# Optimization experiments

Measured on AMD Instinct MI355X. Metric: run time of the kernel, lower is better.

Reference implementation:

```python
import jax, jax.numpy as jnp
import numpy as np

N_LVL = [131072, 32768, 8192, 2048, 512, 256]  # active voxels per pyramid level
B = 8          # point clouds in batch
K = 27         # 3x3x3 kernel offsets
SLOPE = 0.01   # LeakyReLU default negative slope
EPS = 1e-5     # BatchNorm eps


def _bn(x, g, b):
    # MinkowskiBatchNorm, training-mode forward: stats over all points
    m = x.mean(0)
    v = x.var(0)
    return (x - m) * jax.lax.rsqrt(v + EPS) * g + b


def _lrelu(x):
    return jnp.where(x >= 0, x, SLOPE * x)


def _lin_block(x, w, g, b):
    # MinkowskiLinear(bias=False) + BN + LeakyReLU (also models 1x1 conv)
    return _lrelu(_bn(x @ w, g, b))


def _conv_block(x, nbr, w, g, b):
    # sparse conv as gather-GEMM: [N,K,Cin] x [K,Cin,Cout] -> [N,Cout]
    y = jnp.einsum('nkc,kco->no', x[nbr], w)
    return _lrelu(_bn(y, g, b))


def _maxpool(x, pmap):
    # stride-2 kernel-3 sparse max pool via precomputed pooling map
    return x[pmap].max(axis=1)


def setup_inputs() -> dict:
    key = jax.random.key(0)
    ks = iter(jax.random.split(key, 80))

    def nrm(shape, scale):
        return jax.random.normal(next(ks), shape, dtype=jnp.float32) * jnp.float32(scale)

    inp = {}
    inp['x'] = nrm((N_LVL[0], 3), 1.0)
    inp['w_mlp1'] = nrm((3, 16), 1.0 / np.sqrt(3.0))
    inp['g_mlp1'] = jnp.ones(16, jnp.float32)
    inp['b_mlp1'] = jnp.zeros(16, jnp.float32)
    conv_dims = [(16, 32), (32, 48), (48, 96), (96, 128), (128, 256), (256, 512)]
    down_dims = [(48, 32), (80, 48), (144, 96), (224, 128), (384, 256)]
    for i, (ci, co) in enumerate(conv_dims):
        inp[f'w_c{i+1}'] = nrm((K, ci, co), np.sqrt(2.0 / (K * co)))  # kaiming fan_out
        inp[f'g_c{i+1}'] = jnp.ones(co, jnp.float32)
        inp[f'b_c{i+1}'] = jnp.zeros(co, jnp.float32)
    for i, (ci, co) in enumerate(down_dims):
        inp[f'w_d{i+1}'] = nrm((ci, co), np.sqrt(2.0 / co))
        inp[f'g_d{i+1}'] = jnp.ones(co, jnp.float32)
        inp[f'b_d{i+1}'] = jnp.zeros(co, jnp.float32)
    inp['w_f1'] = nrm((1024, 512), 1.0 / 32.0)
    inp['g_f1'] = jnp.ones(512, jnp.float32)
    inp['b_f1'] = jnp.zeros(512, jnp.float32)
    inp['w_f2'] = nrm((512, 256), 1.0 / np.sqrt(512.0))
    inp['g_f2'] = jnp.ones(256, jnp.float32)
    inp['b_f2'] = jnp.zeros(256, jnp.float32)
    inp['w_f3'] = nrm((256, 20), 1.0 / 16.0)
    inp['bias_f3'] = jnp.zeros(20, jnp.float32)
    for i in range(6):
        inp[f'nbr{i}'] = jax.random.randint(next(ks), (N_LVL[i], K), 0, N_LVL[i], dtype=jnp.int32)
    for i in range(1, 6):
        inp[f'pool{i}'] = jax.random.randint(next(ks), (N_LVL[i], K), 0, N_LVL[i - 1], dtype=jnp.int32)
    inp['batch5'] = jnp.repeat(jnp.arange(B, dtype=jnp.int32), N_LVL[5] // B)
    return inp


def reference(x, w_mlp1, g_mlp1, b_mlp1,
              w_c1, g_c1, b_c1, w_c2, g_c2, b_c2, w_c3, g_c3, b_c3,
              w_c4, g_c4, b_c4, w_c5, g_c5, b_c5, w_c6, g_c6, b_c6,
              w_d1, g_d1, b_d1, w_d2, g_d2, b_d2, w_d3, g_d3, b_d3,
              w_d4, g_d4, b_d4, w_d5, g_d5, b_d5,
              w_f1, g_f1, b_f1, w_f2, g_f2, b_f2, w_f3, bias_f3,
              nbr0, nbr1, nbr2, nbr3, nbr4, nbr5,
              pool1, pool2, pool3, pool4, pool5, batch5):
    convs = [(w_c1, g_c1, b_c1), (w_c2, g_c2, b_c2), (w_c3, g_c3, b_c3),
             (w_c4, g_c4, b_c4), (w_c5, g_c5, b_c5)]
    downs = [(w_d1, g_d1, b_d1), (w_d2, g_d2, b_d2), (w_d3, g_d3, b_d3),
             (w_d4, g_d4, b_d4), (w_d5, g_d5, b_d5)]
    nbrs = [nbr0, nbr1, nbr2, nbr3, nbr4]
    pools = [pool1, pool2, pool3, pool4, pool5]

    y = _lin_block(x, w_mlp1, g_mlp1, b_mlp1)  # mlp1, level 0
    for i in range(5):  # fixed 5 conv/cat/down/pool stages (structural loop)
        out = _conv_block(y, nbrs[i], *convs[i])
        y = _lin_block(jnp.concatenate([y, out], axis=1), *downs[i])  # cat + down (1x1)
        y = _maxpool(y, pools[i])
    y = _conv_block(y, nbr5, w_c6, g_c6, b_c6)  # conv6 at level 5: [N5, 512]

    xmax = jax.ops.segment_max(y, batch5, num_segments=B)
    cnt = jax.ops.segment_sum(jnp.ones((y.shape[0], 1), y.dtype), batch5, num_segments=B)
    xavg = jax.ops.segment_sum(y, batch5, num_segments=B) / cnt
    z = jnp.concatenate([xmax, xavg], axis=1)  # [B, 1024]

    z = _lin_block(z, w_f1, g_f1, b_f1)  # dropout = identity (eval)
    z = _lin_block(z, w_f2, g_f2, b_f2)
    return z @ w_f3 + bias_f3  # [B, 20] logits
```

## Files before the change

kernel.cpp:

```cpp
#include <hip/hip_runtime.h>
#include <math.h>

#define BN_EPS 1e-5f


__device__ __forceinline__ void fma4(float s, const float4& w, float4& a) {
    a.x = fmaf(s, w.x, a.x);
    a.y = fmaf(s, w.y, a.y);
    a.z = fmaf(s, w.z, a.z);
    a.w = fmaf(s, w.w, a.w);
}

__device__ __forceinline__ float nlr(float x, float sc, float sh) {
    float t = fmaf(x, sc, sh);
    return fmaxf(t, 0.01f * t);
}

__device__ __forceinline__ void bn_coef(const float* __restrict__ sums,
                                        const float* __restrict__ g,
                                        const float* __restrict__ b,
                                        int C, int c, float inv_n,
                                        float& sc, float& sh) {
    float mean = sums[c] * inv_n;
    float var = fmaxf(fmaf(-mean, mean, sums[C + c] * inv_n), 0.f);
    sc = g[c] * rsqrtf(var + BN_EPS);
    sh = fmaf(-mean, sc, b[c]);
}

__global__ void zero_kernel(float* __restrict__ p, int n) {
    int i = blockIdx.x * blockDim.x + threadIdx.x;
    if (i < n) p[i] = 0.f;
}

__global__ __launch_bounds__(256) void mlp1s_kernel(
    const float* __restrict__ x, const float* __restrict__ w,
    float* __restrict__ out, int N, float* __restrict__ sums) {
    __shared__ float ls[32];
    int tid = threadIdx.x;
    if (tid < 32) ls[tid] = 0.f;
    __syncthreads();
    int n = blockIdx.x * blockDim.x + tid;
    float o[16];
    if (n < N) {
        float x0 = x[n * 3], x1 = x[n * 3 + 1], x2 = x[n * 3 + 2];
        #pragma unroll
        for (int c = 0; c < 16; c++)
            o[c] = fmaf(x0, w[c], fmaf(x1, w[16 + c], x2 * w[32 + c]));
        #pragma unroll
        for (int c4 = 0; c4 < 4; c4++)
            *reinterpret_cast<float4*>(out + n * 16 + c4 * 4) =
                make_float4(o[c4 * 4], o[c4 * 4 + 1], o[c4 * 4 + 2], o[c4 * 4 + 3]);
    } else {
        #pragma unroll
        for (int c = 0; c < 16; c++) o[c] = 0.f;
    }
    float q[16];
    #pragma unroll
    for (int c = 0; c < 16; c++) q[c] = o[c] * o[c];
    #pragma unroll
    for (int m = 1; m < 64; m <<= 1) {
        #pragma unroll
        for (int c = 0; c < 16; c++) {
            o[c] += __shfl_xor(o[c], m, 64);
            q[c] += __shfl_xor(q[c], m, 64);
        }
    }
    if ((tid & 63) == 0) {
        #pragma unroll
        for (int c = 0; c < 16; c++) {
            atomicAdd(&ls[c], o[c]);
            atomicAdd(&ls[16 + c], q[c]);
        }
    }
    __syncthreads();
    if (tid < 32) atomicAdd(&sums[tid], ls[tid]);
}

__global__ void norm0_kernel(float4* __restrict__ y, int total4,
                             const float* __restrict__ sums, const float* __restrict__ g,
                             const float* __restrict__ b, float inv_n) {
    __shared__ float lsc[16], lsh[16];
    int tid = threadIdx.x;
    if (tid < 16) {
        float sc, sh;
        bn_coef(sums, g, b, 16, tid, inv_n, sc, sh);
        lsc[tid] = sc;
        lsh[tid] = sh;
    }
    __syncthreads();
    int i = blockIdx.x * blockDim.x + tid;
    if (i >= total4) return;
    int cb = (i & 3) * 4;
    float4 v = y[i];
    v.x = nlr(v.x, lsc[cb + 0], lsh[cb + 0]);
    v.y = nlr(v.y, lsc[cb + 1], lsh[cb + 1]);
    v.z = nlr(v.z, lsc[cb + 2], lsh[cb + 2]);
    v.w = nlr(v.w, lsc[cb + 3], lsh[cb + 3]);
    y[i] = v;
}

__global__ void stats4_kernel(const float4* __restrict__ x, int total4, int C, int C4,
                              float* __restrict__ sums) {
    __shared__ float ls[1024];
    int tid = threadIdx.x;
    for (int j = tid; j < 2 * C; j += blockDim.x) ls[j] = 0.f;
    __syncthreads();
    int stride = gridDim.x * blockDim.x;
    int i = blockIdx.x * blockDim.x + tid;
    int c4 = i % C4;
    float4 s = make_float4(0.f, 0.f, 0.f, 0.f);
    float4 q = make_float4(0.f, 0.f, 0.f, 0.f);
    for (; i < total4; i += stride) {
        float4 v = x[i];
        s.x += v.x; s.y += v.y; s.z += v.z; s.w += v.w;
        q.x = fmaf(v.x, v.x, q.x); q.y = fmaf(v.y, v.y, q.y);
        q.z = fmaf(v.z, v.z, q.z); q.w = fmaf(v.w, v.w, q.w);
    }
    int cb = c4 * 4;
    atomicAdd(&ls[cb + 0], s.x); atomicAdd(&ls[cb + 1], s.y);
    atomicAdd(&ls[cb + 2], s.z); atomicAdd(&ls[cb + 3], s.w);
    atomicAdd(&ls[C + cb + 0], q.x); atomicAdd(&ls[C + cb + 1], q.y);
    atomicAdd(&ls[C + cb + 2], q.z); atomicAdd(&ls[C + cb + 3], q.w);
    __syncthreads();
    for (int j = tid; j < 2 * C; j += blockDim.x) atomicAdd(&sums[j], ls[j]);
}

template <int C, int KS>
__global__ void reducek_kernel(const float4* __restrict__ in, float4* __restrict__ out,
                               int total4, float* __restrict__ sums) {
    __shared__ float ls[1024];
    constexpr int C4 = C / 4;
    int tid = threadIdx.x;
    for (int j = tid; j < 2 * C; j += blockDim.x) ls[j] = 0.f;
    __syncthreads();
    int stride = gridDim.x * blockDim.x;
    int i = blockIdx.x * blockDim.x + tid;
    int c4 = i % C4;
    float4 s = make_float4(0.f, 0.f, 0.f, 0.f);
    float4 q = make_float4(0.f, 0.f, 0.f, 0.f);
    for (; i < total4; i += stride) {
        float4 v = make_float4(0.f, 0.f, 0.f, 0.f);
        #pragma unroll
        for (int p = 0; p < KS; p++) {
            float4 t = in[(size_t)p * total4 + i];
            v.x += t.x; v.y += t.y; v.z += t.z; v.w += t.w;
        }
        out[i] = v;
        s.x += v.x; s.y += v.y; s.z += v.z; s.w += v.w;
        q.x = fmaf(v.x, v.x, q.x); q.y = fmaf(v.y, v.y, q.y);
        q.z = fmaf(v.z, v.z, q.z); q.w = fmaf(v.w, v.w, q.w);
    }
    int cb = c4 * 4;
    atomicAdd(&ls[cb + 0], s.x); atomicAdd(&ls[cb + 1], s.y);
    atomicAdd(&ls[cb + 2], s.z); atomicAdd(&ls[cb + 3], s.w);
    atomicAdd(&ls[C + cb + 0], q.x); atomicAdd(&ls[C + cb + 1], q.y);
    atomicAdd(&ls[C + cb + 2], q.z); atomicAdd(&ls[C + cb + 3], q.w);
    __syncthreads();
    for (int j = tid; j < 2 * C; j += blockDim.x) atomicAdd(&sums[j], ls[j]);
}

template <int CIN, int COUT, int CO_TILE, int NCOT, int MT, int TM, int NTHR,
          int NQ, int KT, bool STATS, bool PREF>
__global__ __launch_bounds__(NTHR) void convd_kernel(
    const float* __restrict__ y, const int* __restrict__ nbr,
    const float* __restrict__ w, float* __restrict__ out,
    float* __restrict__ s_out) {
    constexpr int CQT = CO_TILE / (4 * NQ);
    constexpr int MGRP = NTHR / CQT;
    constexpr int RT = TM / MGRP;
    constexpr int C4N = CIN / 4;
    static_assert(MGRP * RT == TM, "tile mismatch");
    static_assert(MGRP * CQT == NTHR, "thread mismatch");

    __shared__ float sred[STATS ? 2 * CO_TILE : 1];

    const int tid = threadIdx.x;
    const int bid = blockIdx.x;
    const int cot = bid % NCOT;
    const int rest = bid / NCOT;
    const int mt = rest % MT;
    const int ks = rest / MT;
    const int m0 = mt * TM;
    const int cobase = cot * CO_TILE;
    const int k0 = ks * KT;
    const int cq = tid % CQT;
    const int mg = tid / CQT;

    int mrow[RT];
    #pragma unroll
    for (int r = 0; r < RT; r++) mrow[r] = m0 + mg + r * MGRP;

    float4 acc[RT][NQ];
    #pragma unroll
    for (int r = 0; r < RT; r++)
        #pragma unroll
        for (int q = 0; q < NQ; q++) acc[r][q] = make_float4(0.f, 0.f, 0.f, 0.f);

    auto ldidx = [&](int k, int (&rr)[RT]) {
        #pragma unroll
        for (int r = 0; r < RT; r++) rr[r] = nbr[(size_t)mrow[r] * 27 + k];
    };

    if constexpr (PREF) {
        auto ldy = [&](const int (&rr)[RT], float4 (&yv)[RT][C4N]) {
            #pragma unroll
            for (int r = 0; r < RT; r++)
                #pragma unroll
                for (int c4 = 0; c4 < C4N; c4++)
                    yv[r][c4] = *reinterpret_cast<const float4*>(
                        y + (size_t)rr[r] * CIN + c4 * 4);
        };
        auto fmak = [&](int k, const float4 (&yv)[RT][C4N]) {
            const float* wk = w + (size_t)k * CIN * COUT + cobase + cq * (4 * NQ);
            #pragma unroll
            for (int c4 = 0; c4 < C4N; c4++) {
                #pragma unroll
                for (int jj = 0; jj < 4; jj++) {
                    #pragma unroll
                    for (int q = 0; q < NQ; q++) {
                        float4 wv = *reinterpret_cast<const float4*>(
                            wk + (size_t)(c4 * 4 + jj) * COUT + q * 4);
                        #pragma unroll
                        for (int r = 0; r < RT; r++) {
                            float e = jj == 0 ? yv[r][c4].x : jj == 1 ? yv[r][c4].y
                                     : jj == 2 ? yv[r][c4].z : yv[r][c4].w;
                            fma4(e, wv, acc[r][q]);
                        }
                    }
                }
            }
        };
        int ra[RT], rb[RT];
        float4 ya[RT][C4N], yb[RT][C4N];
        ldidx(k0, ra);
        ldy(ra, ya);
        int kk = 0;
        for (; kk + 2 <= KT; kk += 2) {
            ldidx(k0 + kk + 1, rb);
            ldy(rb, yb);
            fmak(k0 + kk, ya);
            if (kk + 2 < KT) {
                ldidx(k0 + kk + 2, ra);
                ldy(ra, ya);
            }
            fmak(k0 + kk + 1, yb);
        }
        if (KT & 1) fmak(k0 + KT - 1, ya);
    } else {
        int rows[RT];
        ldidx(k0, rows);
        for (int kk = k0; kk < k0 + KT; kk++) {
            int rnext[RT];
            if (kk + 1 < k0 + KT) ldidx(kk + 1, rnext);
            const float* wk = w + (size_t)kk * CIN * COUT + cobase + cq * (4 * NQ);
            #pragma unroll 4
            for (int c4 = 0; c4 < C4N; c4++) {
                float4 yv[RT];
                #pragma unroll
                for (int r = 0; r < RT; r++)
                    yv[r] = *reinterpret_cast<const float4*>(
                        y + (size_t)rows[r] * CIN + c4 * 4);
                #pragma unroll
                for (int jj = 0; jj < 4; jj++) {
                    #pragma unroll
                    for (int q = 0; q < NQ; q++) {
                        float4 wv = *reinterpret_cast<const float4*>(
                            wk + (size_t)(c4 * 4 + jj) * COUT + q * 4);
                        #pragma unroll
                        for (int r = 0; r < RT; r++) {
                            float e = jj == 0 ? yv[r].x : jj == 1 ? yv[r].y
                                     : jj == 2 ? yv[r].z : yv[r].w;
                            fma4(e, wv, acc[r][q]);
                        }
                    }
                }
            }
            #pragma unroll
            for (int r = 0; r < RT; r++) rows[r] = rnext[r];
        }
    }

    float* outp = out + (size_t)ks * MT * TM * COUT;
    #pragma unroll
    for (int r = 0; r < RT; r++)
        #pragma unroll
        for (int q = 0; q < NQ; q++)
            *reinterpret_cast<float4*>(
                outp + (size_t)mrow[r] * COUT + cobase + cq * (4 * NQ) + q * 4) =
                acc[r][q];

    if constexpr (STATS) {
        for (int j = tid; j < 2 * CO_TILE; j += NTHR) sred[j] = 0.f;
        __syncthreads();
        #pragma unroll
        for (int q = 0; q < NQ; q++) {
            float4 s = make_float4(0.f, 0.f, 0.f, 0.f);
            float4 qq = make_float4(0.f, 0.f, 0.f, 0.f);
            #pragma unroll
            for (int r = 0; r < RT; r++) {
                float4 v = acc[r][q];
                s.x += v.x; s.y += v.y; s.z += v.z; s.w += v.w;
                qq.x = fmaf(v.x, v.x, qq.x); qq.y = fmaf(v.y, v.y, qq.y);
                qq.z = fmaf(v.z, v.z, qq.z); qq.w = fmaf(v.w, v.w, qq.w);
            }
            int cb = cq * (4 * NQ) + q * 4;
            atomicAdd(&sred[cb + 0], s.x); atomicAdd(&sred[cb + 1], s.y);
            atomicAdd(&sred[cb + 2], s.z); atomicAdd(&sred[cb + 3], s.w);
            atomicAdd(&sred[CO_TILE + cb + 0], qq.x);
            atomicAdd(&sred[CO_TILE + cb + 1], qq.y);
            atomicAdd(&sred[CO_TILE + cb + 2], qq.z);
            atomicAdd(&sred[CO_TILE + cb + 3], qq.w);
        }
        __syncthreads();
        for (int j = tid; j < CO_TILE; j += NTHR) {
            atomicAdd(&s_out[cobase + j], sred[j]);
            atomicAdd(&s_out[COUT + cobase + j], sred[CO_TILE + j]);
        }
    }
}

template <int C1, int C2, int COUT, int NQ, int NTHR>
__global__ __launch_bounds__(NTHR) void down3_kernel(
    const float* __restrict__ in1, const float* __restrict__ in2,
    const float* __restrict__ w, float* __restrict__ out,
    const float* __restrict__ s2, const float* __restrict__ g2,
    const float* __restrict__ b2, float inv2,
    float* __restrict__ s_out) {
    constexpr int CQT = COUT / (4 * NQ);
    constexpr int PAIRS = NTHR / CQT;
    __shared__ __align__(16) float n2c[C2], n2h[C2];
    __shared__ float sred[2 * COUT];

    const int tid = threadIdx.x;
    for (int c = tid; c < C2; c += NTHR) {
        float sc, sh;
        bn_coef(s2, g2, b2, C2, c, inv2, sc, sh);
        n2c[c] = sc; n2h[c] = sh;
    }
    for (int j = tid; j < 2 * COUT; j += NTHR) sred[j] = 0.f;
    __syncthreads();

    const int cq = tid % CQT;
    const int pr = tid / CQT;
    const int n0 = (blockIdx.x * PAIRS + pr) * 2;

    float4 acc[2][NQ];
    #pragma unroll
    for (int r = 0; r < 2; r++)
        #pragma unroll
        for (int q = 0; q < NQ; q++) acc[r][q] = make_float4(0.f, 0.f, 0.f, 0.f);

    const float* w1 = w + cq * (4 * NQ);
    #pragma unroll 8
    for (int ci4 = 0; ci4 < C1 / 4; ci4++) {
        float4 a0 = *reinterpret_cast<const float4*>(in1 + (size_t)n0 * C1 + ci4 * 4);
        float4 a1 = *reinterpret_cast<const float4*>(in1 + (size_t)(n0 + 1) * C1 + ci4 * 4);
        #pragma unroll
        for (int jj = 0; jj < 4; jj++) {
            const float* wp = w1 + (size_t)(ci4 * 4 + jj) * COUT;
            float e0 = jj == 0 ? a0.x : jj == 1 ? a0.y : jj == 2 ? a0.z : a0.w;
            float e1 = jj == 0 ? a1.x : jj == 1 ? a1.y : jj == 2 ? a1.z : a1.w;
            #pragma unroll
            for (int q = 0; q < NQ; q++) {
                float4 wv = *reinterpret_cast<const float4*>(wp + q * 4);
                fma4(e0, wv, acc[0][q]);
                fma4(e1, wv, acc[1][q]);
            }
        }
    }
    const float* w2 = w + (size_t)C1 * COUT + cq * (4 * NQ);
    #pragma unroll 8
    for (int ci4 = 0; ci4 < C2 / 4; ci4++) {
        float4 a0 = *reinterpret_cast<const float4*>(in2 + (size_t)n0 * C2 + ci4 * 4);
        float4 a1 = *reinterpret_cast<const float4*>(in2 + (size_t)(n0 + 1) * C2 + ci4 * 4);
        float4 sc = *reinterpret_cast<const float4*>(&n2c[ci4 * 4]);
        float4 sh = *reinterpret_cast<const float4*>(&n2h[ci4 * 4]);
        a0.x = nlr(a0.x, sc.x, sh.x); a0.y = nlr(a0.y, sc.y, sh.y);
        a0.z = nlr(a0.z, sc.z, sh.z); a0.w = nlr(a0.w, sc.w, sh.w);
        a1.x = nlr(a1.x, sc.x, sh.x); a1.y = nlr(a1.y, sc.y, sh.y);
        a1.z = nlr(a1.z, sc.z, sh.z); a1.w = nlr(a1.w, sc.w, sh.w);
        #pragma unroll
        for (int jj = 0; jj < 4; jj++) {
            const float* wp = w2 + (size_t)(ci4 * 4 + jj) * COUT;
            float e0 = jj == 0 ? a0.x : jj == 1 ? a0.y : jj == 2 ? a0.z : a0.w;
            float e1 = jj == 0 ? a1.x : jj == 1 ? a1.y : jj == 2 ? a1.z : a1.w;
            #pragma unroll
            for (int q = 0; q < NQ; q++) {
                float4 wv = *reinterpret_cast<const float4*>(wp + q * 4);
                fma4(e0, wv, acc[0][q]);
                fma4(e1, wv, acc[1][q]);
            }
        }
    }
    #pragma unroll
    for (int r = 0; r < 2; r++)
        #pragma unroll
        for (int q = 0; q < NQ; q++)
            *reinterpret_cast<float4*>(out + (size_t)(n0 + r) * COUT + cq * (4 * NQ) + q * 4) =
                acc[r][q];

    #pragma unroll
    for (int q = 0; q < NQ; q++) {
        float4 s = make_float4(0.f, 0.f, 0.f, 0.f);
        float4 qq = make_float4(0.f, 0.f, 0.f, 0.f);
        #pragma unroll
        for (int r = 0; r < 2; r++) {
            float4 v = acc[r][q];
            s.x += v.x; s.y += v.y; s.z += v.z; s.w += v.w;
            qq.x = fmaf(v.x, v.x, qq.x); qq.y = fmaf(v.y, v.y, qq.y);
            qq.z = fmaf(v.z, v.z, qq.z); qq.w = fmaf(v.w, v.w, qq.w);
        }
        int cb = cq * (4 * NQ) + q * 4;
        atomicAdd(&sred[cb + 0], s.x); atomicAdd(&sred[cb + 1], s.y);
        atomicAdd(&sred[cb + 2], s.z); atomicAdd(&sred[cb + 3], s.w);
        atomicAdd(&sred[COUT + cb + 0], qq.x);
        atomicAdd(&sred[COUT + cb + 1], qq.y);
        atomicAdd(&sred[COUT + cb + 2], qq.z);
        atomicAdd(&sred[COUT + cb + 3], qq.w);
    }
    __syncthreads();
    for (int j = tid; j < COUT; j += NTHR) {
        atomicAdd(&s_out[j], sred[j]);
        atomicAdd(&s_out[COUT + j], sred[COUT + j]);
    }
}

template <int C, int NTHR>
__global__ __launch_bounds__(NTHR) void pool2_kernel(
    const float* __restrict__ draw, const int* __restrict__ pmap,
    const float* __restrict__ sums, const float* __restrict__ g,
    const float* __restrict__ b, float inv_n,
    float* __restrict__ yout, int Nout) {
    constexpr int C4 = C / 4;
    int i = blockIdx.x * NTHR + threadIdx.x;
    if (i >= Nout * C4) return;
    int n = i / C4, c4 = i % C4;
    float sc[4], sh[4];
    #pragma unroll
    for (int j = 0; j < 4; j++) bn_coef(sums, g, b, C, c4 * 4 + j, inv_n, sc[j], sh[j]);
    const int* pm = pmap + n * 27;
    float4 mn = make_float4(INFINITY, INFINITY, INFINITY, INFINITY);
    float4 mx = make_float4(-INFINITY, -INFINITY, -INFINITY, -INFINITY);
    #pragma unroll 9
    for (int k = 0; k < 27; k++) {
        int row = pm[k];
        float4 v = *reinterpret_cast<const float4*>(draw + (size_t)row * C + c4 * 4);
        mn.x = fminf(mn.x, v.x); mn.y = fminf(mn.y, v.y);
        mn.z = fminf(mn.z, v.z); mn.w = fminf(mn.w, v.w);
        mx.x = fmaxf(mx.x, v.x); mx.y = fmaxf(mx.y, v.y);
        mx.z = fmaxf(mx.z, v.z); mx.w = fmaxf(mx.w, v.w);
    }
    float4 o;
    o.x = nlr(sc[0] >= 0.f ? mx.x : mn.x, sc[0], sh[0]);
    o.y = nlr(sc[1] >= 0.f ? mx.y : mn.y, sc[1], sh[1]);
    o.z = nlr(sc[2] >= 0.f ? mx.z : mn.z, sc[2], sh[2]);
    o.w = nlr(sc[3] >= 0.f ? mx.w : mn.w, sc[3], sh[3]);
    *reinterpret_cast<float4*>(yout + (size_t)n * C + c4 * 4) = o;
}

__global__ void segpool2_kernel(const float* __restrict__ y,
                                const float* __restrict__ sums,
                                const float* __restrict__ g, const float* __restrict__ b,
                                float inv_n, float* __restrict__ z) {
    int bi = blockIdx.x;
    int c = threadIdx.x;
    float sc, sh;
    bn_coef(sums, g, b, 512, c, inv_n, sc, sh);
    float mn = INFINITY, mx = -INFINITY, sm = 0.f;
    for (int r = 0; r < 32; r++) {
        float v = y[(size_t)(bi * 32 + r) * 512 + c];
        mn = fminf(mn, v);
        mx = fmaxf(mx, v);
        sm += nlr(v, sc, sh);
    }
    z[bi * 1024 + c] = nlr(sc >= 0.f ? mx : mn, sc, sh);
    z[bi * 1024 + 512 + c] = sm * (1.f / 32.f);
}

template <int K, int COUT, int KSPLIT, bool NORM>
__global__ __launch_bounds__(256) void fc_kernel(
    const float* __restrict__ z, const float* __restrict__ w,
    const float* __restrict__ ns, const float* __restrict__ ng,
    const float* __restrict__ nb, float inv_n,
    float* __restrict__ out) {
    constexpr int KC = K / KSPLIT;
    constexpr int KG = KC / 16;
    __shared__ __align__(16) float zt[KC * 8];
    __shared__ float red[16 * 520];

    const int cobase = blockIdx.x * 64;
    const int kc0 = blockIdx.y * KC;
    const int tid = threadIdx.x;
    const int coq = tid & 15;
    const int kg = tid >> 4;

    for (int idx = tid; idx < 8 * (KC / 4); idx += 256) {
        int n = idx / (KC / 4);
        int kq = idx - n * (KC / 4);
        float4 v = *reinterpret_cast<const float4*>(z + (size_t)n * K + kc0 + kq * 4);
        if constexpr (NORM) {
            #pragma unroll
            for (int j = 0; j < 4; j++) {
                float sc, sh;
                bn_coef(ns, ng, nb, K, kc0 + kq * 4 + j, inv_n, sc, sh);
                float* pv = j == 0 ? &v.x : j == 1 ? &v.y : j == 2 ? &v.z : &v.w;
                *pv = nlr(*pv, sc, sh);
            }
        }
        zt[(kq * 4 + 0) * 8 + n] = v.x;
        zt[(kq * 4 + 1) * 8 + n] = v.y;
        zt[(kq * 4 + 2) * 8 + n] = v.z;
        zt[(kq * 4 + 3) * 8 + n] = v.w;
    }
    __syncthreads();

    float4 acc[8];
    #pragma unroll
    for (int n = 0; n < 8; n++) acc[n] = make_float4(0.f, 0.f, 0.f, 0.f);
    for (int ki = 0; ki < KG; ki++) {
        int k = kg * KG + ki;
        float4 wv = *reinterpret_cast<const float4*>(
            w + (size_t)(kc0 + k) * COUT + cobase + coq * 4);
        float4 za = *reinterpret_cast<const float4*>(&zt[k * 8]);
        float4 zb = *reinterpret_cast<const float4*>(&zt[k * 8 + 4]);
        fma4(za.x, wv, acc[0]); fma4(za.y, wv, acc[1]);
        fma4(za.z, wv, acc[2]); fma4(za.w, wv, acc[3]);
        fma4(zb.x, wv, acc[4]); fma4(zb.y, wv, acc[5]);
        fma4(zb.z, wv, acc[6]); fma4(zb.w, wv, acc[7]);
    }
    #pragma unroll
    for (int n = 0; n < 8; n++) {
        red[kg * 520 + (coq * 4 + 0) * 8 + n] = acc[n].x;
        red[kg * 520 + (coq * 4 + 1) * 8 + n] = acc[n].y;
        red[kg * 520 + (coq * 4 + 2) * 8 + n] = acc[n].z;
        red[kg * 520 + (coq * 4 + 3) * 8 + n] = acc[n].w;
    }
    __syncthreads();
    for (int oi = tid; oi < 512; oi += 256) {
        int c = oi >> 3;
        int n = oi & 7;
        float s = 0.f;
        #pragma unroll
        for (int gg = 0; gg < 16; gg++) s += red[gg * 520 + c * 8 + n];
        float* op = out + (size_t)n * COUT + cobase + c;
        if (KSPLIT > 1) atomicAdd(op, s);
        else *op = s;
    }
}

__global__ void f3n_kernel(const float* __restrict__ in, const float* __restrict__ w,
                           const float* __restrict__ bias,
                           const float* __restrict__ sums, const float* __restrict__ g,
                           const float* __restrict__ b, float inv_n,
                           float* __restrict__ out) {
    __shared__ float zin[8 * 256];
    int tid = threadIdx.x;
    for (int idx = tid; idx < 2048; idx += 256) {
        int c = idx & 255;
        float sc, sh;
        bn_coef(sums, g, b, 256, c, inv_n, sc, sh);
        zin[idx] = nlr(in[idx], sc, sh);
    }
    __syncthreads();
    if (tid >= 160) return;
    int n = tid / 20, co = tid % 20;
    float acc = bias[co];
    for (int ci = 0; ci < 256; ci++)
        acc = fmaf(zin[n * 256 + ci], w[ci * 20 + co], acc);
    out[tid] = acc;
}


extern "C" void kernel_launch(void* const* d_in, const int* in_sizes, int n_in,
                              void* d_out, int out_size, void* d_ws, size_t ws_size,
                              hipStream_t stream) {
    (void)in_sizes; (void)n_in; (void)out_size; (void)ws_size;

    const int N0 = 131072, N1 = 32768, N2 = 8192, N3 = 2048, N4 = 512, N5 = 256;

    const float* x      = (const float*)d_in[0];
    const float* w_mlp1 = (const float*)d_in[1];
    const float* g_mlp1 = (const float*)d_in[2];
    const float* b_mlp1 = (const float*)d_in[3];
    const float* w_c[6]; const float* g_c[6]; const float* b_c[6];
    for (int i = 0; i < 6; i++) {
        w_c[i] = (const float*)d_in[4 + 3 * i];
        g_c[i] = (const float*)d_in[5 + 3 * i];
        b_c[i] = (const float*)d_in[6 + 3 * i];
    }
    const float* w_d[5]; const float* g_d[5]; const float* b_d[5];
    for (int i = 0; i < 5; i++) {
        w_d[i] = (const float*)d_in[22 + 3 * i];
        g_d[i] = (const float*)d_in[23 + 3 * i];
        b_d[i] = (const float*)d_in[24 + 3 * i];
    }
    const float* w_f1 = (const float*)d_in[37];
    const float* g_f1 = (const float*)d_in[38];
    const float* b_f1 = (const float*)d_in[39];
    const float* w_f2 = (const float*)d_in[40];
    const float* g_f2 = (const float*)d_in[41];
    const float* b_f2 = (const float*)d_in[42];
    const float* w_f3 = (const float*)d_in[43];
    const float* bias_f3 = (const float*)d_in[44];
    const int* nbr[6];
    for (int i = 0; i < 6; i++) nbr[i] = (const int*)d_in[45 + i];
    const int* pool[5];
    for (int i = 0; i < 5; i++) pool[i] = (const int*)d_in[51 + i];

    float* ws    = (float*)d_ws;
    float* bufA  = ws;
    float* bufB  = bufA + 2097152;
    float* bufC  = bufB + 4194304;
    float* stats = bufC + 4194304;
    float* out = (float*)d_out;

    auto st = [&](int slot) { return stats + slot * 1024; };

    const float iN0 = 1.f / N0, iN1 = 1.f / N1, iN2 = 1.f / N2, iN3 = 1.f / N3,
                iN4 = 1.f / N4, iN5 = 1.f / N5, i8 = 1.f / 8.f;

    zero_kernel<<<56, 256, 0, stream>>>(stats, 14 * 1024);

    mlp1s_kernel<<<N0 / 256, 256, 0, stream>>>(x, w_mlp1, bufA, N0, st(0));
    norm0_kernel<<<N0 * 4 / 256, 256, 0, stream>>>(
        (float4*)bufA, N0 * 4, st(0), g_mlp1, b_mlp1, iN0);

    convd_kernel<16, 32, 32, 1, 2048, 64, 256, 2, 27, true, true>
        <<<2048, 256, 0, stream>>>(bufA, nbr[0], w_c[0], bufB, st(1));
    down3_kernel<16, 32, 32, 2, 256>
        <<<1024, 256, 0, stream>>>(bufA, bufB, w_d[0], bufC,
                                   st(1), g_c[0], b_c[0], iN0, st(2));
    pool2_kernel<32, 256><<<N1 * 8 / 256, 256, 0, stream>>>(
        bufC, pool[0], st(2), g_d[0], b_d[0], iN0, bufA, N1);

    convd_kernel<32, 48, 48, 1, 512, 64, 192, 2, 9, false, false>
        <<<1536, 192, 0, stream>>>(bufA, nbr[1], w_c[1], bufB, nullptr);
    reducek_kernel<48, 3><<<1024, 192, 0, stream>>>(
        (const float4*)bufB, (float4*)bufB, N1 * 12, st(3));
    down3_kernel<32, 48, 48, 2, 192>
        <<<512, 192, 0, stream>>>(bufA, bufB, w_d[1], bufC,
                                  st(3), g_c[1], b_c[1], iN1, st(4));
    pool2_kernel<48, 192><<<N2 * 12 / 192, 192, 0, stream>>>(
        bufC, pool[1], st(4), g_d[1], b_d[1], iN1, bufA, N2);

    convd_kernel<48, 96, 48, 2, 128, 64, 192, 2, 3, false, false>
        <<<2304, 192, 0, stream>>>(bufA, nbr[2], w_c[2], bufB, nullptr);
    reducek_kernel<96, 9><<<1024, 192, 0, stream>>>(
        (const float4*)bufB, (float4*)bufB, N2 * 24, st(5));
    down3_kernel<48, 96, 96, 2, 192>
        <<<256, 192, 0, stream>>>(bufA, bufB, w_d[2], bufC,
                                  st(5), g_c[2], b_c[2], iN2, st(6));
    pool2_kernel<96, 192><<<N3 * 24 / 192, 192, 0, stream>>>(
        bufC, pool[2], st(6), g_d[2], b_d[2], iN2, bufA, N3);

    convd_kernel<96, 128, 64, 2, 32, 64, 256, 2, 1, false, false>
        <<<1728, 256, 0, stream>>>(bufA, nbr[3], w_c[3], bufB, nullptr);
    reducek_kernel<128, 27><<<256, 256, 0, stream>>>(
        (const float4*)bufB, (float4*)bufB, N3 * 32, st(7));
    down3_kernel<96, 128, 128, 2, 256>
        <<<64, 256, 0, stream>>>(bufA, bufB, w_d[3], bufC,
                                 st(7), g_c[3], b_c[3], iN3, st(8));
    pool2_kernel<128, 256><<<N4 * 32 / 256, 256, 0, stream>>>(
        bufC, pool[3], st(8), g_d[3], b_d[3], iN3, bufA, N4);

    convd_kernel<128, 256, 64, 4, 8, 64, 256, 2, 1, false, false>
        <<<864, 256, 0, stream>>>(bufA, nbr[4], w_c[4], bufB, nullptr);
    reducek_kernel<256, 27><<<128, 256, 0, stream>>>(
        (const float4*)bufB, (float4*)bufB, N4 * 64, st(9));
    down3_kernel<128, 256, 256, 2, 256>
        <<<32, 256, 0, stream>>>(bufA, bufB, w_d[4], bufC,
                                 st(9), g_c[4], b_c[4], iN4, st(10));
    pool2_kernel<256, 256><<<N5 * 64 / 256, 256, 0, stream>>>(
        bufC, pool[4], st(10), g_d[4], b_d[4], iN4, bufA, N5);

    convd_kernel<256, 512, 64, 8, 4, 64, 256, 2, 1, false, false>
        <<<864, 256, 0, stream>>>(bufA, nbr[5], w_c[5], bufB, nullptr);
    reducek_kernel<512, 27><<<128, 256, 0, stream>>>(
        (const float4*)bufB, (float4*)bufB, N5 * 128, st(11));

    segpool2_kernel<<<8, 512, 0, stream>>>(bufB, st(11), g_c[5], b_c[5], iN5, bufC);

    zero_kernel<<<16, 256, 0, stream>>>(bufB, 4096);
    fc_kernel<1024, 512, 4, false><<<dim3(8, 4), 256, 0, stream>>>(
        bufC, w_f1, nullptr, nullptr, nullptr, 0.f, bufB);
    stats4_kernel<<<4, 256, 0, stream>>>((const float4*)bufB, 1024, 512, 128, st(12));

    zero_kernel<<<8, 256, 0, stream>>>(bufB + 4096, 2048);
    fc_kernel<512, 256, 4, true><<<dim3(4, 4), 256, 0, stream>>>(
        bufB, w_f2, st(12), g_f1, b_f1, i8, bufB + 4096);
    stats4_kernel<<<2, 256, 0, stream>>>(
        (const float4*)(bufB + 4096), 512, 256, 64, st(13));

    f3n_kernel<<<1, 256, 0, stream>>>(bufB + 4096, w_f3, bias_f3,
                                      st(13), g_f2, b_f2, i8, out);
}
```

Measured before the change: 1.063 ms.

## Split level-0 features into channel halves for narrower gather rows in conv1

The normalized level-0 features are written as two 8-channel planes instead of one 16-channel array. A dedicated conv1 kernel then runs twice, once per half, so each neighbor gather reads 32 bytes instead of 64. The two partial outputs are summed by reducek, which also gathers the BN stats. A specialised down1 kernel reads from the split layout. The aim is better cache locality for the random 27-neighbor gathers, at the cost of an extra launch, a reduction pass and an extra partial buffer. The generic convd loses its PREF prefetch path, which is now unused.

New measurement: 1.097 ms. 3.2% more time.

```diff
diff --git a/kernel.cpp b/kernel.cpp
--- a/kernel.cpp
+++ b/kernel.cpp
@@ -76,9 +76,11 @@
     if (tid < 32) atomicAdd(&sums[tid], ls[tid]);
 }
 
-__global__ void norm0_kernel(float4* __restrict__ y, int total4,
-                             const float* __restrict__ sums, const float* __restrict__ g,
-                             const float* __restrict__ b, float inv_n) {
+__global__ void norm0s_kernel(const float* __restrict__ in,
+                              float* __restrict__ lo, float* __restrict__ hi,
+                              int N, const float* __restrict__ sums,
+                              const float* __restrict__ g, const float* __restrict__ b,
+                              float inv_n) {
     __shared__ float lsc[16], lsh[16];
     int tid = threadIdx.x;
     if (tid < 16) {
@@ -88,15 +90,22 @@
         lsh[tid] = sh;
     }
     __syncthreads();
-    int i = blockIdx.x * blockDim.x + tid;
-    if (i >= total4) return;
-    int cb = (i & 3) * 4;
-    float4 v = y[i];
-    v.x = nlr(v.x, lsc[cb + 0], lsh[cb + 0]);
-    v.y = nlr(v.y, lsc[cb + 1], lsh[cb + 1]);
-    v.z = nlr(v.z, lsc[cb + 2], lsh[cb + 2]);
-    v.w = nlr(v.w, lsc[cb + 3], lsh[cb + 3]);
-    y[i] = v;
+    int n = blockIdx.x * blockDim.x + tid;
+    if (n >= N) return;
+    const float4* row = reinterpret_cast<const float4*>(in + (size_t)n * 16);
+    float4 v0 = row[0], v1 = row[1], v2 = row[2], v3 = row[3];
+    v0.x = nlr(v0.x, lsc[0], lsh[0]);   v0.y = nlr(v0.y, lsc[1], lsh[1]);
+    v0.z = nlr(v0.z, lsc[2], lsh[2]);   v0.w = nlr(v0.w, lsc[3], lsh[3]);
+    v1.x = nlr(v1.x, lsc[4], lsh[4]);   v1.y = nlr(v1.y, lsc[5], lsh[5]);
+    v1.z = nlr(v1.z, lsc[6], lsh[6]);   v1.w = nlr(v1.w, lsc[7], lsh[7]);
+    v2.x = nlr(v2.x, lsc[8], lsh[8]);   v2.y = nlr(v2.y, lsc[9], lsh[9]);
+    v2.z = nlr(v2.z, lsc[10], lsh[10]); v2.w = nlr(v2.w, lsc[11], lsh[11]);
+    v3.x = nlr(v3.x, lsc[12], lsh[12]); v3.y = nlr(v3.y, lsc[13], lsh[13]);
+    v3.z = nlr(v3.z, lsc[14], lsh[14]); v3.w = nlr(v3.w, lsc[15], lsh[15]);
+    float4* lp = reinterpret_cast<float4*>(lo + (size_t)n * 8);
+    float4* hp = reinterpret_cast<float4*>(hi + (size_t)n * 8);
+    lp[0] = v0; lp[1] = v1;
+    hp[0] = v2; hp[1] = v3;
 }
 
 __global__ void stats4_kernel(const float4* __restrict__ x, int total4, int C, int C4,
@@ -159,8 +168,160 @@
     for (int j = tid; j < 2 * C; j += blockDim.x) atomicAdd(&sums[j], ls[j]);
 }
 
+__global__ __launch_bounds__(256) void conv1s_kernel(
+    const float* __restrict__ y, const int* __restrict__ nbr,
+    const float* __restrict__ wb, float* __restrict__ out) {
+    const int tid = threadIdx.x;
+    const int mrow = blockIdx.x * 64 + (tid >> 2);
+    const int cq = tid & 3;
+    const int* nb = nbr + (size_t)mrow * 27;
+
+    float4 acc0 = make_float4(0.f, 0.f, 0.f, 0.f);
+    float4 acc1 = make_float4(0.f, 0.f, 0.f, 0.f);
+
+    auto fmak = [&](int k, float4 u0, float4 u1) {
+        const float* wk = wb + k * 512 + cq * 8;
+        float f[8] = {u0.x, u0.y, u0.z, u0.w, u1.x, u1.y, u1.z, u1.w};
+        #pragma unroll
+        for (int ci = 0; ci < 8; ci++) {
+            float4 wv0 = *reinterpret_cast<const float4*>(wk + ci * 32);
+            float4 wv1 = *reinterpret_cast<const float4*>(wk + ci * 32 + 4);
+            fma4(f[ci], wv0, acc0);
+            fma4(f[ci], wv1, acc1);
+        }
+    };
+
+    int ra = nb[0];
+    float4 a0 = *reinterpret_cast<const float4*>(y + (size_t)ra * 8);
+    float4 a1 = *reinterpret_cast<const float4*>(y + (size_t)ra * 8 + 4);
+    #pragma unroll
+    for (int kk = 0; kk + 2 <= 27; kk += 2) {
+        int rb = nb[kk + 1];
+        float4 b0 = *reinterpret_cast<const float4*>(y + (size_t)rb * 8);
+        float4 b1 = *reinterpret_cast<const float4*>(y + (size_t)rb * 8 + 4);
+        fmak(kk, a0, a1);
+        if (kk + 2 < 27) {
+            ra = nb[kk + 2];
+            a0 = *reinterpret_cast<const float4*>(y + (size_t)ra * 8);
+            a1 = *reinterpret_cast<const float4*>(y + (size_t)ra * 8 + 4);
+        }
+        fmak(kk + 1, b0, b1);
+    }
+    fmak(26, a0, a1);
+
+    *reinterpret_cast<float4*>(out + (size_t)mrow * 32 + cq * 8) = acc0;
+    *reinterpret_cast<float4*>(out + (size_t)mrow * 32 + cq * 8 + 4) = acc1;
+}
+
+__global__ __launch_bounds__(256) void down1s_kernel(
+    const float* __restrict__ lo, const float* __restrict__ hi,
+    const float* __restrict__ in2, const float* __restrict__ w,
+    float* __restrict__ out,
+    const float* __restrict__ s2, const float* __restrict__ g2,
+    const float* __restrict__ b2, float inv2,
+    float* __restrict__ s_out) {
+    constexpr int C2 = 32, COUT = 32;
+    __shared__ __align__(16) float n2c[C2], n2h[C2];
+    __shared__ float sred[2 * COUT];
+
+    const int tid = threadIdx.x;
+    if (tid < C2) {
+        float sc, sh;
+        bn_coef(s2, g2, b2, C2, tid, inv2, sc, sh);
+        n2c[tid] = sc; n2h[tid] = sh;
+    }
+    for (int j = tid; j < 2 * COUT; j += 256) sred[j] = 0.f;
+    __syncthreads();
+
+    const int cq = tid & 3;
+    const int pr = tid >> 2;
+    const int n0 = (blockIdx.x * 64 + pr) * 2;
+
+    float4 acc[2][2];
+    #pragma unroll
+    for (int r = 0; r < 2; r++)
+        #pragma unroll
+        for (int q = 0; q < 2; q++) acc[r][q] = make_float4(0.f, 0.f, 0.f, 0.f);
+
+    const float* w1 = w + cq * 8;
+    #pragma unroll
+    for (int half = 0; half < 2; half++) {
+        const float* src = half == 0 ? lo : hi;
+        float4 a00 = *reinterpret_cast<const float4*>(src + (size_t)n0 * 8);
+        float4 a01 = *reinterpret_cast<const float4*>(src + (size_t)n0 * 8 + 4);
+        float4 a10 = *reinterpret_cast<const float4*>(src + (size_t)(n0 + 1) * 8);
+        float4 a11 = *reinterpret_cast<const float4*>(src + (size_t)(n0 + 1) * 8 + 4);
+        float e0[8] = {a00.x, a00.y, a00.z, a00.w, a01.x, a01.y, a01.z, a01.w};
+        float e1[8] = {a10.x, a10.y, a10.z, a10.w, a11.x, a11.y, a11.z, a11.w};
+        #pragma unroll
+        for (int jj = 0; jj < 8; jj++) {
+            const float* wp = w1 + (size_t)(half * 8 + jj) * COUT;
+            float4 wv0 = *reinterpret_cast<const float4*>(wp);
+            float4 wv1 = *reinterpret_cast<const float4*>(wp + 4);
+            fma4(e0[jj], wv0, acc[0][0]);
+            fma4(e0[jj], wv1, acc[0][1]);
+            fma4(e1[jj], wv0, acc[1][0]);
+            fma4(e1[jj], wv1, acc[1][1]);
+        }
+    }
+    const float* w2 = w + 16 * COUT + cq * 8;
+    #pragma unroll
+    for (int ci4 = 0; ci4 < C2 / 4; ci4++) {
+        float4 a0 = *reinterpret_cast<const float4*>(in2 + (size_t)n0 * C2 + ci4 * 4);
+        float4 a1 = *reinterpret_cast<const float4*>(in2 + (size_t)(n0 + 1) * C2 + ci4 * 4);
+        float4 sc = *reinterpret_cast<const float4*>(&n2c[ci4 * 4]);
+        float4 sh = *reinterpret_cast<const float4*>(&n2h[ci4 * 4]);
+        a0.x = nlr(a0.x, sc.x, sh.x); a0.y = nlr(a0.y, sc.y, sh.y);
+        a0.z = nlr(a0.z, sc.z, sh.z); a0.w = nlr(a0.w, sc.w, sh.w);
+        a1.x = nlr(a1.x, sc.x, sh.x); a1.y = nlr(a1.y, sc.y, sh.y);
+        a1.z = nlr(a1.z, sc.z, sh.z); a1.w = nlr(a1.w, sc.w, sh.w);
+        #pragma unroll
+        for (int jj = 0; jj < 4; jj++) {
+            const float* wp = w2 + (size_t)(ci4 * 4 + jj) * COUT;
+            float4 wv0 = *reinterpret_cast<const float4*>(wp);
+            float4 wv1 = *reinterpret_cast<const float4*>(wp + 4);
+            float e0 = jj == 0 ? a0.x : jj == 1 ? a0.y : jj == 2 ? a0.z : a0.w;
+            float e1 = jj == 0 ? a1.x : jj == 1 ? a1.y : jj == 2 ? a1.z : a1.w;
+            fma4(e0, wv0, acc[0][0]);
+            fma4(e0, wv1, acc[0][1]);
+            fma4(e1, wv0, acc[1][0]);
+            fma4(e1, wv1, acc[1][1]);
+        }
+    }
+    #pragma unroll
+    for (int r = 0; r < 2; r++) {
+        *reinterpret_cast<float4*>(out + (size_t)(n0 + r) * COUT + cq * 8) = acc[r][0];
+        *reinterpret_cast<float4*>(out + (size_t)(n0 + r) * COUT + cq * 8 + 4) = acc[r][1];
+    }
+
+    #pragma unroll
+    for (int q = 0; q < 2; q++) {
+        float4 s = make_float4(0.f, 0.f, 0.f, 0.f);
+        float4 qq = make_float4(0.f, 0.f, 0.f, 0.f);
+        #pragma unroll
+        for (int r = 0; r < 2; r++) {
+            float4 v = acc[r][q];
+            s.x += v.x; s.y += v.y; s.z += v.z; s.w += v.w;
+            qq.x = fmaf(v.x, v.x, qq.x); qq.y = fmaf(v.y, v.y, qq.y);
+            qq.z = fmaf(v.z, v.z, qq.z); qq.w = fmaf(v.w, v.w, qq.w);
+        }
+        int cb = cq * 8 + q * 4;
+        atomicAdd(&sred[cb + 0], s.x); atomicAdd(&sred[cb + 1], s.y);
+        atomicAdd(&sred[cb + 2], s.z); atomicAdd(&sred[cb + 3], s.w);
+        atomicAdd(&sred[COUT + cb + 0], qq.x);
+        atomicAdd(&sred[COUT + cb + 1], qq.y);
+        atomicAdd(&sred[COUT + cb + 2], qq.z);
+        atomicAdd(&sred[COUT + cb + 3], qq.w);
+    }
+    __syncthreads();
+    for (int j = tid; j < COUT; j += 256) {
+        atomicAdd(&s_out[j], sred[j]);
+        atomicAdd(&s_out[COUT + j], sred[COUT + j]);
+    }
+}
+
 template <int CIN, int COUT, int CO_TILE, int NCOT, int MT, int TM, int NTHR,
-          int NQ, int KT, bool STATS, bool PREF>
+          int NQ, int KT, bool STATS>
 __global__ __launch_bounds__(NTHR) void convd_kernel(
     const float* __restrict__ y, const int* __restrict__ nbr,
     const float* __restrict__ w, float* __restrict__ out,
@@ -201,83 +362,36 @@
         for (int r = 0; r < RT; r++) rr[r] = nbr[(size_t)mrow[r] * 27 + k];
     };
 
-    if constexpr (PREF) {
-        auto ldy = [&](const int (&rr)[RT], float4 (&yv)[RT][C4N]) {
+    int rows[RT];
+    ldidx(k0, rows);
+    for (int kk = k0; kk < k0 + KT; kk++) {
+        int rnext[RT];
+        if (kk + 1 < k0 + KT) ldidx(kk + 1, rnext);
+        const float* wk = w + (size_t)kk * CIN * COUT + cobase + cq * (4 * NQ);
+        #pragma unroll 4
+        for (int c4 = 0; c4 < C4N; c4++) {
+            float4 yv[RT];
             #pragma unroll
             for (int r = 0; r < RT; r++)
+                yv[r] = *reinterpret_cast<const float4*>(
+                    y + (size_t)rows[r] * CIN + c4 * 4);
+            #pragma unroll
+            for (int jj = 0; jj < 4; jj++) {
                 #pragma unroll
-                for (int c4 = 0; c4 < C4N; c4++)
-                    yv[r][c4] = *reinterpret_cast<const float4*>(
-                        y + (size_t)rr[r] * CIN + c4 * 4);
-        };
-        auto fmak = [&](int k, const float4 (&yv)[RT][C4N]) {
-            const float* wk = w + (size_t)k * CIN * COUT + cobase + cq * (4 * NQ);
-            #pragma unroll
-            for (int c4 = 0; c4 < C4N; c4++) {
-                #pragma unroll
-                for (int jj = 0; jj < 4; jj++) {
+                for (int q = 0; q < NQ; q++) {
+                    float4 wv = *reinterpret_cast<const float4*>(
+                        wk + (size_t)(c4 * 4 + jj) * COUT + q * 4);
                     #pragma unroll
-                    for (int q = 0; q < NQ; q++) {
-                        float4 wv = *reinterpret_cast<const float4*>(
-                            wk + (size_t)(c4 * 4 + jj) * COUT + q * 4);
-                        #pragma unroll
-                        for (int r = 0; r < RT; r++) {
-                            float e = jj == 0 ? yv[r][c4].x : jj == 1 ? yv[r][c4].y
-                                     : jj == 2 ? yv[r][c4].z : yv[r][c4].w;
-                            fma4(e, wv, acc[r][q]);
-                        }
+                    for (int r = 0; r < RT; r++) {
+                        float e = jj == 0 ? yv[r].x : jj == 1 ? yv[r].y
+                                 : jj == 2 ? yv[r].z : yv[r].w;
+                        fma4(e, wv, acc[r][q]);
                     }
                 }
             }
-        };
-        int ra[RT], rb[RT];
-        float4 ya[RT][C4N], yb[RT][C4N];
-        ldidx(k0, ra);
-        ldy(ra, ya);
-        int kk = 0;
-        for (; kk + 2 <= KT; kk += 2) {
-            ldidx(k0 + kk + 1, rb);
-            ldy(rb, yb);
-            fmak(k0 + kk, ya);
-            if (kk + 2 < KT) {
-                ldidx(k0 + kk + 2, ra);
-                ldy(ra, ya);
-            }
-            fmak(k0 + kk + 1, yb);
-        }
-        if (KT & 1) fmak(k0 + KT - 1, ya);
-    } else {
-        int rows[RT];
-        ldidx(k0, rows);
-        for (int kk = k0; kk < k0 + KT; kk++) {
-            int rnext[RT];
-            if (kk + 1 < k0 + KT) ldidx(kk + 1, rnext);
-            const float* wk = w + (size_t)kk * CIN * COUT + cobase + cq * (4 * NQ);
-            #pragma unroll 4
-            for (int c4 = 0; c4 < C4N; c4++) {
-                float4 yv[RT];
-                #pragma unroll
-                for (int r = 0; r < RT; r++)
-                    yv[r] = *reinterpret_cast<const float4*>(
-                        y + (size_t)rows[r] * CIN + c4 * 4);
-                #pragma unroll
-                for (int jj = 0; jj < 4; jj++) {
-                    #pragma unroll
-                    for (int q = 0; q < NQ; q++) {
-                        float4 wv = *reinterpret_cast<const float4*>(
-                            wk + (size_t)(c4 * 4 + jj) * COUT + q * 4);
-                        #pragma unroll
-                        for (int r = 0; r < RT; r++) {
-                            float e = jj == 0 ? yv[r].x : jj == 1 ? yv[r].y
-                                     : jj == 2 ? yv[r].z : yv[r].w;
-                            fma4(e, wv, acc[r][q]);
-                        }
-                    }
-                }
-            }
-            #pragma unroll
-            for (int r = 0; r < RT; r++) rows[r] = rnext[r];
-        }
+        }
+        #pragma unroll
+        for (int r = 0; r < RT; r++) rows[r] = rnext[r];
     }
 
     float* outp = out + (size_t)ks * MT * TM * COUT;
@@ -612,6 +726,8 @@
     float* bufB  = bufA + 2097152;
     float* bufC  = bufB + 4194304;
     float* stats = bufC + 4194304;
+    float* y0lo  = bufA;
+    float* y0hi  = bufA + 1048576;
     float* out = (float*)d_out;
 
     auto st = [&](int slot) { return stats + slot * 1024; };
@@ -621,19 +737,20 @@
 
     zero_kernel<<<56, 256, 0, stream>>>(stats, 14 * 1024);
 
-    mlp1s_kernel<<<N0 / 256, 256, 0, stream>>>(x, w_mlp1, bufA, N0, st(0));
-    norm0_kernel<<<N0 * 4 / 256, 256, 0, stream>>>(
-        (float4*)bufA, N0 * 4, st(0), g_mlp1, b_mlp1, iN0);
-
-    convd_kernel<16, 32, 32, 1, 2048, 64, 256, 2, 27, true, true>
-        <<<2048, 256, 0, stream>>>(bufA, nbr[0], w_c[0], bufB, st(1));
-    down3_kernel<16, 32, 32, 2, 256>
-        <<<1024, 256, 0, stream>>>(bufA, bufB, w_d[0], bufC,
-                                   st(1), g_c[0], b_c[0], iN0, st(2));
+    mlp1s_kernel<<<N0 / 256, 256, 0, stream>>>(x, w_mlp1, bufB, N0, st(0));
+    norm0s_kernel<<<N0 / 256, 256, 0, stream>>>(
+        bufB, y0lo, y0hi, N0, st(0), g_mlp1, b_mlp1, iN0);
+
+    conv1s_kernel<<<N0 / 64, 256, 0, stream>>>(y0lo, nbr[0], w_c[0], bufB);
+    conv1s_kernel<<<N0 / 64, 256, 0, stream>>>(y0hi, nbr[0], w_c[0] + 256, bufC);
+    reducek_kernel<32, 2><<<1024, 256, 0, stream>>>(
+        (const float4*)bufB, (float4*)bufB, N0 * 8, st(1));
+    down1s_kernel<<<N0 / 128, 256, 0, stream>>>(
+        y0lo, y0hi, bufB, w_d[0], bufC, st(1), g_c[0], b_c[0], iN0, st(2));
     pool2_kernel<32, 256><<<N1 * 8 / 256, 256, 0, stream>>>(
         bufC, pool[0], st(2), g_d[0], b_d[0], iN0, bufA, N1);
 
-    convd_kernel<32, 48, 48, 1, 512, 64, 192, 2, 9, false, false>
+    convd_kernel<32, 48, 48, 1, 512, 64, 192, 2, 9, false>
         <<<1536, 192, 0, stream>>>(bufA, nbr[1], w_c[1], bufB, nullptr);
     reducek_kernel<48, 3><<<1024, 192, 0, stream>>>(
         (const float4*)bufB, (float4*)bufB, N1 * 12, st(3));
@@ -643,7 +760,7 @@
     pool2_kernel<48, 192><<<N2 * 12 / 192, 192, 0, stream>>>(
         bufC, pool[1], st(4), g_d[1], b_d[1], iN1, bufA, N2);
 
-    convd_kernel<48, 96, 48, 2, 128, 64, 192, 2, 3, false, false>
+    convd_kernel<48, 96, 48, 2, 128, 64, 192, 2, 3, false>
         <<<2304, 192, 0, stream>>>(bufA, nbr[2], w_c[2], bufB, nullptr);
     reducek_kernel<96, 9><<<1024, 192, 0, stream>>>(
         (const float4*)bufB, (float4*)bufB, N2 * 24, st(5));
@@ -653,7 +770,7 @@
     pool2_kernel<96, 192><<<N3 * 24 / 192, 192, 0, stream>>>(
         bufC, pool[2], st(6), g_d[2], b_d[2], iN2, bufA, N3);
 
-    convd_kernel<96, 128, 64, 2, 32, 64, 256, 2, 1, false, false>
+    convd_kernel<96, 128, 64, 2, 32, 64, 256, 2, 1, false>
         <<<1728, 256, 0, stream>>>(bufA, nbr[3], w_c[3], bufB, nullptr);
     reducek_kernel<128, 27><<<256, 256, 0, stream>>>(
         (const float4*)bufB, (float4*)bufB, N3 * 32, st(7));
@@ -663,7 +780,7 @@
     pool2_kernel<128, 256><<<N4 * 32 / 256, 256, 0, stream>>>(
         bufC, pool[3], st(8), g_d[3], b_d[3], iN3, bufA, N4);
 
-    convd_kernel<128, 256, 64, 4, 8, 64, 256, 2, 1, false, false>
+    convd_kernel<128, 256, 64, 4, 8, 64, 256, 2, 1, false>
         <<<864, 256, 0, stream>>>(bufA, nbr[4], w_c[4], bufB, nullptr);
     reducek_kernel<256, 27><<<128, 256, 0, stream>>>(
         (const float4*)bufB, (float4*)bufB, N4 * 64, st(9));
@@ -673,7 +790,7 @@
     pool2_kernel<256, 256><<<N5 * 64 / 256, 256, 0, stream>>>(
         bufC, pool[4], st(10), g_d[4], b_d[4], iN4, bufA, N5);
 
-    convd_kernel<256, 512, 64, 8, 4, 64, 256, 2, 1, false, false>
+    convd_kernel<256, 512, 64, 8, 4, 64, 256, 2, 1, false>
         <<<864, 256, 0, stream>>>(bufA, nbr[5], w_c[5], bufB, nullptr);
     reducek_kernel<512, 27><<<128, 256, 0, stream>>>(
         (const float4*)bufB, (float4*)bufB, N5 * 128, st(11));
```
